# Kernel optimization log

Hardware: AMD Instinct MI355X
Metric: run time of the kernel (lower is better)

The kernel has to match this reference:

```python
import jax, jax.numpy as jnp
import numpy as np

B, T, C, H = 8, 1024, 1024, 16
NEG = -1000000000.0
EPS = 1e-12


def setup_inputs() -> dict:
    key = jax.random.key(0)
    ks = jax.random.split(key, 12)
    s = 0.02  # keep pre-softmax logits in a sane range
    return {
        "x": jax.random.normal(ks[0], (B, T, C), jnp.float32),
        "mask": jax.random.randint(ks[1], (B, T), 0, 2, jnp.int32),
        "Wq": jax.random.normal(ks[2], (C, C), jnp.float32) * s,
        "bq": jax.random.normal(ks[3], (C,), jnp.float32) * s,
        "Wk": jax.random.normal(ks[4], (C, C), jnp.float32) * s,
        "bk": jax.random.normal(ks[5], (C,), jnp.float32) * s,
        "Wv": jax.random.normal(ks[6], (C, C), jnp.float32) * s,
        "bv": jax.random.normal(ks[7], (C,), jnp.float32) * s,
        "Wp": jax.random.normal(ks[8], (C, C), jnp.float32) * s,
        "bp": jax.random.normal(ks[9], (C,), jnp.float32) * s,
        "ln_w": jnp.ones((C,), jnp.float32),
        "ln_b": jnp.zeros((C,), jnp.float32),
    }


def reference(x, mask, Wq, bq, Wk, bk, Wv, bv, Wp, bp, ln_w, ln_b):
    Bx, Tx, Cx = x.shape
    hd = Cx // H
    # torch nn.Linear: y = x @ W.T + b
    def lin(inp, W, b):
        return inp @ W.T + b

    def split_heads(t):  # [B,T,C] -> [B,H,T,hd]
        return t.reshape(Bx, Tx, H, hd).transpose(0, 2, 1, 3)

    q = split_heads(lin(x, Wq, bq))
    k = split_heads(lin(x, Wk, bk))
    v = split_heads(lin(x, Wv, bv))

    att = jnp.einsum("bhqd,bhkd->bhqk", q, k) * (1.0 / jnp.sqrt(jnp.float32(hd)))
    # mask [B,T] masks key positions; broadcast to [B,1,1,T]
    att = jnp.where(mask[:, None, None, :] == 0, NEG, att)
    # stable softmax (manual max-subtract, matching original)
    att = jax.nn.softmax(att, axis=-1)
    # dropout prob 0.0 -> identity (eval-mode faithful)
    y = jnp.einsum("bhqk,bhkd->bhqd", att, v)
    y = y.transpose(0, 2, 1, 3).reshape(Bx, Tx, Cx)
    y = lin(y, Wp, bp)
    # residual + LayerNorm(eps=1e-12)
    z = y + x
    mu = jnp.mean(z, axis=-1, keepdims=True)
    var = jnp.mean(jnp.square(z - mu), axis=-1, keepdims=True)
    out = (z - mu) * jax.lax.rsqrt(var + EPS) * ln_w + ln_b
    return out
```

## Files before the change

### kernel.cpp

```cpp
#include <hip/hip_runtime.h>
#include <stdint.h>

#define B_ 8
#define T_ 1024
#define C_ 1024
#define H_ 16
#define HD 64
#define M_TOT (B_ * T_)

using f32x4 = __attribute__((ext_vector_type(4))) float;
using s16x8 = __attribute__((ext_vector_type(8))) short;
using i32x4 = __attribute__((ext_vector_type(4))) int;

__device__ __forceinline__ unsigned short f2bf(float f) {
  unsigned int u = __builtin_bit_cast(unsigned int, f);
  unsigned int r = (u + 0x7fffu + ((u >> 16) & 1u)) >> 16;
  return (unsigned short)r;
}

__device__ __forceinline__ void gload_lds16(const void* g, void* l) {
  __builtin_amdgcn_global_load_lds(
      (const __attribute__((address_space(1))) unsigned int*)g,
      (__attribute__((address_space(3))) unsigned int*)l, 16, 0, 0);
}

__global__ __launch_bounds__(256) void k_convert(
    const float* __restrict__ x, const float* __restrict__ wq,
    const float* __restrict__ wk, const float* __restrict__ wv,
    const float* __restrict__ wp, const float* __restrict__ bq,
    const float* __restrict__ bk, const float* __restrict__ bv,
    const int* __restrict__ maskp, unsigned short* __restrict__ xb,
    unsigned short* __restrict__ wqkv, unsigned short* __restrict__ wpb,
    float* __restrict__ bias_cat, unsigned int* __restrict__ mpair) {
  const long n_x = (long)M_TOT * C_;
  const long W_ELT = (long)C_ * C_;
  const long total4 = (n_x + 4 * W_ELT) >> 2;
  for (long i4 = (long)blockIdx.x * blockDim.x + threadIdx.x; i4 < total4;
       i4 += (long)gridDim.x * blockDim.x) {
    long i = i4 << 2;
    const float* src;
    unsigned short* dst;
    if (i < n_x) {
      src = x + i;
      dst = xb + i;
    } else {
      long off = i - n_x;
      int which = (int)(off >> 20);
      long wo = off & (W_ELT - 1);
      if (which < 3) {
        src = (which == 0 ? wq : which == 1 ? wk : wv) + wo;
        dst = wqkv + which * W_ELT + wo;
      } else {
        src = wp + wo;
        dst = wpb + wo;
      }
    }
    float4 v = *(const float4*)src;
    ushort4 u;
    u.x = f2bf(v.x); u.y = f2bf(v.y); u.z = f2bf(v.z); u.w = f2bf(v.w);
    *(ushort4*)dst = u;
  }
  int t = blockIdx.x * blockDim.x + threadIdx.x;
  if (t < 3 * C_) {
    float v = t < C_ ? bq[t] : (t < 2 * C_ ? bk[t - C_] : bv[t - 2 * C_]);
    bias_cat[t] = v;
  }
  if (t < B_ * T_ / 2) {
    const int* mr = maskp + t * 2;
    mpair[t] = (mr[0] ? 0xFFFFu : 0u) | (mr[1] ? 0xFFFF0000u : 0u);
  }
}

template <int EPI>
__global__ __launch_bounds__(256, 2) void k_gemm(
    const unsigned short* __restrict__ A, const unsigned short* __restrict__ Bm,
    const float* __restrict__ bias, unsigned short* __restrict__ q_ws,
    unsigned short* __restrict__ k_ws, unsigned short* __restrict__ vt_ws,
    const float* __restrict__ xres, float* __restrict__ zout) {
  __shared__ unsigned short Al[2][128 * 64];
  __shared__ unsigned short Bl[2][128 * 64];
  const int tid = threadIdx.x, lane = tid & 63, w = tid >> 6;
  const int lc = lane & 15, lr = lane >> 4;
  const int wm = w >> 1, wn = w & 1;
  const int GX = (EPI == 0) ? 24 : 8;
  const int NWG = GX * 64;
  int flat = blockIdx.y * GX + blockIdx.x;
  int swz = (flat & 7) * (NWG / 8) + (flat >> 3);
  const int m0 = (swz / GX) * 128, n0 = (swz % GX) * 128;
  const char* Ab = (const char*)A;
  const char* Bb = (const char*)Bm;

  f32x4 acc[4][4] = {};

  auto stage = [&](int buf, int kt) {
#pragma unroll
    for (int i = 0; i < 4; ++i) {
      int g = i * 256 + tid;
      int row = g >> 3, gr = g & 7;
      gload_lds16(Ab + (long)(m0 + row) * 2048 + kt * 128 + ((gr ^ (row & 7)) << 4),
                  (char*)Al[buf] + (i * 256 + w * 64) * 16);
    }
#pragma unroll
    for (int i = 0; i < 4; ++i) {
      int g = i * 256 + tid;
      int row = g >> 3, gr = g & 7;
      gload_lds16(Bb + (long)(n0 + row) * 2048 + kt * 128 + ((gr ^ (row & 7)) << 4),
                  (char*)Bl[buf] + (i * 256 + w * 64) * 16);
    }
  };

  stage(0, 0);
  stage(1, 1);
  asm volatile("s_waitcnt vmcnt(8)" ::: "memory");
  __builtin_amdgcn_sched_barrier(0);
  __builtin_amdgcn_s_barrier();
  __builtin_amdgcn_sched_barrier(0);

#pragma unroll
  for (int kt = 0; kt < 16; ++kt) {
    const int cur = kt & 1;
    const char* Ac = (const char*)Al[cur];
    const char* Bc = (const char*)Bl[cur];
    s16x8 af0[4], bf0[4];
#pragma unroll
    for (int mf = 0; mf < 4; ++mf) {
      int ar = wm * 64 + mf * 16 + lc;
      af0[mf] = *(const s16x8*)(Ac + ar * 128 + ((lr ^ (ar & 7)) << 4));
    }
#pragma unroll
    for (int nf = 0; nf < 4; ++nf) {
      int br = wn * 64 + nf * 16 + lc;
      bf0[nf] = *(const s16x8*)(Bc + br * 128 + ((lr ^ (br & 7)) << 4));
    }
#pragma unroll
    for (int mf = 0; mf < 4; ++mf)
#pragma unroll
      for (int nf = 0; nf < 4; ++nf)
        acc[mf][nf] = __builtin_amdgcn_mfma_f32_16x16x32_bf16(af0[mf], bf0[nf],
                                                              acc[mf][nf], 0, 0, 0);
    s16x8 af1[4], bf1[4];
#pragma unroll
    for (int mf = 0; mf < 4; ++mf) {
      int ar = wm * 64 + mf * 16 + lc;
      af1[mf] = *(const s16x8*)(Ac + ar * 128 + (((4 + lr) ^ (ar & 7)) << 4));
    }
#pragma unroll
    for (int nf = 0; nf < 4; ++nf) {
      int br = wn * 64 + nf * 16 + lc;
      bf1[nf] = *(const s16x8*)(Bc + br * 128 + (((4 + lr) ^ (br & 7)) << 4));
    }
    asm volatile("s_waitcnt lgkmcnt(0)" ::: "memory");
    __builtin_amdgcn_sched_barrier(0);
    __builtin_amdgcn_s_barrier();
    __builtin_amdgcn_sched_barrier(0);
    if (kt + 2 < 16) stage(cur, kt + 2);
    __builtin_amdgcn_s_setprio(1);
#pragma unroll
    for (int mf = 0; mf < 4; ++mf)
#pragma unroll
      for (int nf = 0; nf < 4; ++nf)
        acc[mf][nf] = __builtin_amdgcn_mfma_f32_16x16x32_bf16(af1[mf], bf1[nf],
                                                              acc[mf][nf], 0, 0, 0);
    __builtin_amdgcn_s_setprio(0);
    if (kt + 2 < 16)
      asm volatile("s_waitcnt vmcnt(8)" ::: "memory");
    else
      asm volatile("s_waitcnt vmcnt(0)" ::: "memory");
    __builtin_amdgcn_sched_barrier(0);
    __builtin_amdgcn_s_barrier();
    __builtin_amdgcn_sched_barrier(0);
  }

  if (EPI == 0) {
#pragma unroll
    for (int mf = 0; mf < 4; ++mf)
#pragma unroll
      for (int nf = 0; nf < 4; ++nf) {
        int gn = n0 + wn * 64 + nf * 16 + lc;
        int which = gn >> 10, nn = gn & 1023;
        int hh = nn >> 6, dd = nn & 63;
        float bia = bias[gn];
        if (which == 2) {
          int gm = m0 + wm * 64 + mf * 16 + lr * 4;
          int bb = gm >> 10, tt = gm & 1023;
          ushort4 pk;
          pk.x = f2bf(acc[mf][nf][0] + bia);
          pk.y = f2bf(acc[mf][nf][1] + bia);
          pk.z = f2bf(acc[mf][nf][2] + bia);
          pk.w = f2bf(acc[mf][nf][3] + bia);
          *(ushort4*)&vt_ws[((long)(bb * H_ + hh) * HD + dd) * T_ + tt] = pk;
        } else {
          unsigned short* dst = (which == 0) ? q_ws : k_ws;
          float scl = (which == 0) ? 0.18033688011112042f : 1.0f;
#pragma unroll
          for (int i = 0; i < 4; ++i) {
            int gm = m0 + wm * 64 + mf * 16 + lr * 4 + i;
            int bb = gm >> 10, tt = gm & 1023;
            dst[((long)(bb * H_ + hh) * T_ + tt) * HD + dd] =
                f2bf((acc[mf][nf][i] + bia) * scl);
          }
        }
      }
  } else {
#pragma unroll
    for (int mf = 0; mf < 4; ++mf)
#pragma unroll
      for (int nf = 0; nf < 4; ++nf) {
        int gn = n0 + wn * 64 + nf * 16 + lc;
        float bia = bias[gn];
#pragma unroll
        for (int i = 0; i < 4; ++i) {
          int gm = m0 + wm * 64 + mf * 16 + lr * 4 + i;
          long idx = (long)gm * C_ + gn;
          zout[idx] = acc[mf][nf][i] + bia + xres[idx];
        }
      }
  }
}

__global__ __launch_bounds__(512, 4) void k_attn(
    const unsigned short* __restrict__ Qp, const unsigned short* __restrict__ Kp,
    const unsigned short* __restrict__ Vtp, const unsigned int* __restrict__ mpairp,
    unsigned short* __restrict__ Yp) {
  __shared__ unsigned short Kl[2][64 * 64];
  __shared__ unsigned short Vl[2][64 * 64];
  const int tid = threadIdx.x, lane = tid & 63, w = tid >> 6;
  const int bid = blockIdx.x;
  const int xcd = bid & 7, slot = bid >> 3;
  const int bh = xcd * 16 + (slot >> 3);
  const int qt = slot & 7;
  const int b = bh >> 4, h = bh & 15;
  const int lc = lane & 15, lr = lane >> 4;
  const int q0 = qt * 128 + w * 16;

  const unsigned short* qbase = Qp + ((long)bh * T_ + q0) * HD;
  s16x8 aq0 = *(const s16x8*)(qbase + lc * HD + lr * 8);
  s16x8 aq1 = *(const s16x8*)(qbase + lc * HD + 32 + lr * 8);

  s16x8 ones;
#pragma unroll
  for (int j = 0; j < 8; ++j) ones[j] = (short)0x3F80;

  f32x4 o[4] = {};
  f32x4 o_l = {};

  const char* kb_g = (const char*)(Kp + (long)bh * T_ * HD);
  const char* vb_g = (const char*)(Vtp + (long)bh * HD * T_);
  const unsigned int* mrow2 = mpairp + b * (T_ / 2);

  auto stage = [&](int buf, int kt) {
    int f = tid * 16;
    int row = f >> 7;
    int swz = (f & 127) ^ ((row & 7) << 4);
    gload_lds16(kb_g + (long)kt * 8192 + (f & ~127) + swz,
                (char*)Kl[buf] + w * 1024);
    gload_lds16(vb_g + (long)row * (T_ * 2) + kt * 128 + swz,
                (char*)Vl[buf] + w * 1024);
  };

  stage(0, 0);
  __syncthreads();

  const int s01 = lc + ((lane & 16) << 1);
  const int s23 = s01 + 16;
  const bool hi = (lane >= 32);

  int cur = 0;
  for (int kt = 0; kt < T_ / 64; ++kt) {
    if (kt + 1 < T_ / 64) stage(cur ^ 1, kt + 1);

    f32x4 s[4];
    const char* kl = (const char*)Kl[cur];
#pragma unroll
    for (int kf = 0; kf < 4; ++kf) {
      int key = kf * 16 + lc;
      s16x8 kb0 = *(const s16x8*)(kl + ((key * 128 + lr * 16) ^ ((key & 7) << 4)));
      s16x8 kb1 = *(const s16x8*)(kl + ((key * 128 + 64 + lr * 16) ^ ((key & 7) << 4)));
      f32x4 z = {};
      z = __builtin_amdgcn_mfma_f32_16x16x32_bf16(kb0, aq0, z, 0, 0, 0);
      z = __builtin_amdgcn_mfma_f32_16x16x32_bf16(kb1, aq1, z, 0, 0, 0);
      s[kf] = z;
    }

    unsigned int mw[4][2];
#pragma unroll
    for (int kf = 0; kf < 4; ++kf) {
      mw[kf][0] = mrow2[kt * 32 + kf * 8 + lr * 2];
      mw[kf][1] = mrow2[kt * 32 + kf * 8 + lr * 2 + 1];
    }

    unsigned int pk[4][2];
#pragma unroll
    for (int kf = 0; kf < 4; ++kf) {
      float p0 = __builtin_amdgcn_exp2f(s[kf][0]);
      float p1 = __builtin_amdgcn_exp2f(s[kf][1]);
      float p2 = __builtin_amdgcn_exp2f(s[kf][2]);
      float p3 = __builtin_amdgcn_exp2f(s[kf][3]);
      unsigned int u0 = __builtin_bit_cast(unsigned int, p0);
      unsigned int u1 = __builtin_bit_cast(unsigned int, p1);
      unsigned int u2 = __builtin_bit_cast(unsigned int, p2);
      unsigned int u3 = __builtin_bit_cast(unsigned int, p3);
      pk[kf][0] = ((u1 & 0xFFFF0000u) | (u0 >> 16)) & mw[kf][0];
      pk[kf][1] = ((u3 & 0xFFFF0000u) | (u2 >> 16)) & mw[kf][1];
    }

    s16x8 ap[2];
#pragma unroll
    for (int kc = 0; kc < 2; ++kc) {
      unsigned int A0 = pk[kc * 2][0], A1 = pk[kc * 2][1];
      unsigned int B0 = pk[kc * 2 + 1][0], B1 = pk[kc * 2 + 1][1];
      unsigned int w0a = __shfl((int)A0, s01, 64), w0b = __shfl((int)B0, s01, 64);
      unsigned int w1a = __shfl((int)A1, s01, 64), w1b = __shfl((int)B1, s01, 64);
      unsigned int w2a = __shfl((int)A0, s23, 64), w2b = __shfl((int)B0, s23, 64);
      unsigned int w3a = __shfl((int)A1, s23, 64), w3b = __shfl((int)B1, s23, 64);
      i32x4 wv;
      wv[0] = (int)(hi ? w0b : w0a);
      wv[1] = (int)(hi ? w1b : w1a);
      wv[2] = (int)(hi ? w2b : w2a);
      wv[3] = (int)(hi ? w3b : w3a);
      ap[kc] = __builtin_bit_cast(s16x8, wv);
    }

#pragma unroll
    for (int kc = 0; kc < 2; ++kc) {
      int koff = kc * 64 + lr * 16;
      o_l = __builtin_amdgcn_mfma_f32_16x16x32_bf16(ones, ap[kc], o_l, 0, 0, 0);
#pragma unroll
      for (int nf = 0; nf < 4; ++nf) {
        int drow = nf * 16 + lc;
        s16x8 vb = *(const s16x8*)((const char*)Vl[cur] +
                                   ((drow * 128 + koff) ^ ((drow & 7) << 4)));
        o[nf] = __builtin_amdgcn_mfma_f32_16x16x32_bf16(vb, ap[kc], o[nf], 0, 0, 0);
      }
    }
    __syncthreads();
    cur ^= 1;
  }

  float rl = 1.0f / o_l[0];
  unsigned short* yrow = Yp + ((long)(b * T_ + q0 + lc)) * C_ + h * 64;
#pragma unroll
  for (int nf = 0; nf < 4; ++nf) {
    ushort4 pw;
    pw.x = f2bf(o[nf][0] * rl);
    pw.y = f2bf(o[nf][1] * rl);
    pw.z = f2bf(o[nf][2] * rl);
    pw.w = f2bf(o[nf][3] * rl);
    *(ushort4*)(yrow + nf * 16 + lr * 4) = pw;
  }
}

__global__ __launch_bounds__(256) void k_ln(const float* __restrict__ z,
                                            const float* __restrict__ lw,
                                            const float* __restrict__ lb,
                                            float* __restrict__ out) {
  const int row = blockIdx.x;
  float4 v = ((const float4*)(z + (long)row * C_))[threadIdx.x];
  float s = v.x + v.y + v.z + v.w;
  float s2 = v.x * v.x + v.y * v.y + v.z * v.z + v.w * v.w;
#pragma unroll
  for (int d = 1; d < 64; d <<= 1) {
    s += __shfl_xor(s, d, 64);
    s2 += __shfl_xor(s2, d, 64);
  }
  __shared__ float rs[4], rq[4];
  int wv_ = threadIdx.x >> 6;
  if ((threadIdx.x & 63) == 0) { rs[wv_] = s; rq[wv_] = s2; }
  __syncthreads();
  s = rs[0] + rs[1] + rs[2] + rs[3];
  s2 = rq[0] + rq[1] + rq[2] + rq[3];
  float mu = s * (1.0f / C_);
  float var = s2 * (1.0f / C_) - mu * mu;
  float inv = rsqrtf(var + 1e-12f);
  float4 wv4 = ((const float4*)lw)[threadIdx.x];
  float4 bv4 = ((const float4*)lb)[threadIdx.x];
  float4 ov;
  ov.x = (v.x - mu) * inv * wv4.x + bv4.x;
  ov.y = (v.y - mu) * inv * wv4.y + bv4.y;
  ov.z = (v.z - mu) * inv * wv4.z + bv4.z;
  ov.w = (v.w - mu) * inv * wv4.w + bv4.w;
  ((float4*)(out + (long)row * C_))[threadIdx.x] = ov;
}

extern "C" void kernel_launch(void* const* d_in, const int* in_sizes, int n_in,
                              void* d_out, int out_size, void* d_ws,
                              size_t ws_size, hipStream_t stream) {
  const float* x = (const float*)d_in[0];
  const int* mask = (const int*)d_in[1];
  const float* Wq = (const float*)d_in[2];
  const float* bq = (const float*)d_in[3];
  const float* Wk = (const float*)d_in[4];
  const float* bk = (const float*)d_in[5];
  const float* Wv = (const float*)d_in[6];
  const float* bv = (const float*)d_in[7];
  const float* Wp = (const float*)d_in[8];
  const float* bp = (const float*)d_in[9];
  const float* lnw = (const float*)d_in[10];
  const float* lnb = (const float*)d_in[11];
  float* out = (float*)d_out;

  char* ws = (char*)d_ws;
  const size_t MB = 1024 * 1024;
  unsigned short* xb = (unsigned short*)(ws);
  unsigned short* q_ws = (unsigned short*)(ws + 16 * MB);
  unsigned short* k_ws = (unsigned short*)(ws + 32 * MB);
  unsigned short* vt_ws = (unsigned short*)(ws + 48 * MB);
  unsigned short* y_ws = (unsigned short*)(ws + 64 * MB);
  unsigned short* wqkv = (unsigned short*)(ws + 80 * MB);
  unsigned short* wpb = (unsigned short*)(ws + 86 * MB);
  float* bias_cat = (float*)(ws + 88 * MB);
  unsigned int* mpair = (unsigned int*)(ws + 88 * MB + 16384);
  float* z = (float*)(ws);

  k_convert<<<dim3(2048), dim3(256), 0, stream>>>(x, Wq, Wk, Wv, Wp, bq, bk, bv,
                                                  mask, xb, wqkv, wpb, bias_cat,
                                                  mpair);
  k_gemm<0><<<dim3(24, 64), dim3(256), 0, stream>>>(
      xb, wqkv, bias_cat, q_ws, k_ws, vt_ws, nullptr, nullptr);
  k_attn<<<dim3(1024), dim3(512), 0, stream>>>(q_ws, k_ws, vt_ws, mpair, y_ws);
  k_gemm<1><<<dim3(8, 64), dim3(256), 0, stream>>>(
      y_ws, wpb, bp, nullptr, nullptr, nullptr, x, z);
  k_ln<<<dim3(8192), dim3(256), 0, stream>>>(z, lnw, lnb, out);
}
```

Measured before the change: 176.2 us.

## Give each attention wave four query tiles and store the residual sum in bf16

The attention kernel now runs 256-thread blocks in which each wave handles 64 queries (four 16-row groups) instead of 16. Each K/V fragment read from LDS is reused across four MFMAs, halving the number of blocks and cutting LDS traffic per FLOP; s_setprio is added around the PV MFMAs. Separately, the output projection reads the bf16 copy of x as the residual and writes z in bf16, and the LayerNorm reads bf16, halving residual and z memory traffic. This costs more registers per wave (lower occupancy) and rounds the pre-LayerNorm values to bf16, which reduces accuracy.

```diff
diff --git a/kernel.cpp b/kernel.cpp
--- a/kernel.cpp
+++ b/kernel.cpp
@@ -16,6 +16,10 @@
   unsigned int u = __builtin_bit_cast(unsigned int, f);
   unsigned int r = (u + 0x7fffu + ((u >> 16) & 1u)) >> 16;
   return (unsigned short)r;
+}
+__device__ __forceinline__ float bf2f(unsigned short s) {
+  unsigned int u = ((unsigned int)s) << 16;
+  return __builtin_bit_cast(float, u);
 }
 
 __device__ __forceinline__ void gload_lds16(const void* g, void* l) {
@@ -76,7 +80,7 @@
     const unsigned short* __restrict__ A, const unsigned short* __restrict__ Bm,
     const float* __restrict__ bias, unsigned short* __restrict__ q_ws,
     unsigned short* __restrict__ k_ws, unsigned short* __restrict__ vt_ws,
-    const float* __restrict__ xres, float* __restrict__ zout) {
+    const unsigned short* __restrict__ xres16, unsigned short* __restrict__ z16) {
   __shared__ unsigned short Al[2][128 * 64];
   __shared__ unsigned short Bl[2][128 * 64];
   const int tid = threadIdx.x, lane = tid & 63, w = tid >> 6;
@@ -212,13 +216,13 @@
         for (int i = 0; i < 4; ++i) {
           int gm = m0 + wm * 64 + mf * 16 + lr * 4 + i;
           long idx = (long)gm * C_ + gn;
-          zout[idx] = acc[mf][nf][i] + bia + xres[idx];
+          z16[idx] = f2bf(acc[mf][nf][i] + bia + bf2f(xres16[idx]));
         }
       }
   }
 }
 
-__global__ __launch_bounds__(512, 4) void k_attn(
+__global__ __launch_bounds__(256, 2) void k_attn(
     const unsigned short* __restrict__ Qp, const unsigned short* __restrict__ Kp,
     const unsigned short* __restrict__ Vtp, const unsigned int* __restrict__ mpairp,
     unsigned short* __restrict__ Yp) {
@@ -227,35 +231,42 @@
   const int tid = threadIdx.x, lane = tid & 63, w = tid >> 6;
   const int bid = blockIdx.x;
   const int xcd = bid & 7, slot = bid >> 3;
-  const int bh = xcd * 16 + (slot >> 3);
-  const int qt = slot & 7;
+  const int bh = xcd * 16 + (slot >> 2);
+  const int qt = slot & 3;
   const int b = bh >> 4, h = bh & 15;
   const int lc = lane & 15, lr = lane >> 4;
-  const int q0 = qt * 128 + w * 16;
+  const int q0 = qt * 256 + w * 64;
 
   const unsigned short* qbase = Qp + ((long)bh * T_ + q0) * HD;
-  s16x8 aq0 = *(const s16x8*)(qbase + lc * HD + lr * 8);
-  s16x8 aq1 = *(const s16x8*)(qbase + lc * HD + 32 + lr * 8);
+  s16x8 aq[4][2];
+#pragma unroll
+  for (int g = 0; g < 4; ++g) {
+    aq[g][0] = *(const s16x8*)(qbase + (g * 16 + lc) * HD + lr * 8);
+    aq[g][1] = *(const s16x8*)(qbase + (g * 16 + lc) * HD + 32 + lr * 8);
+  }
 
   s16x8 ones;
 #pragma unroll
   for (int j = 0; j < 8; ++j) ones[j] = (short)0x3F80;
 
-  f32x4 o[4] = {};
-  f32x4 o_l = {};
+  f32x4 o[4][4] = {};
+  f32x4 ol[4] = {};
 
   const char* kb_g = (const char*)(Kp + (long)bh * T_ * HD);
   const char* vb_g = (const char*)(Vtp + (long)bh * HD * T_);
   const unsigned int* mrow2 = mpairp + b * (T_ / 2);
 
   auto stage = [&](int buf, int kt) {
-    int f = tid * 16;
-    int row = f >> 7;
-    int swz = (f & 127) ^ ((row & 7) << 4);
-    gload_lds16(kb_g + (long)kt * 8192 + (f & ~127) + swz,
-                (char*)Kl[buf] + w * 1024);
-    gload_lds16(vb_g + (long)row * (T_ * 2) + kt * 128 + swz,
-                (char*)Vl[buf] + w * 1024);
+#pragma unroll
+    for (int it = 0; it < 2; ++it) {
+      int f = it * 4096 + w * 1024 + lane * 16;
+      int row = f >> 7;
+      int swz = (f & 127) ^ ((row & 7) << 4);
+      gload_lds16(kb_g + (long)kt * 8192 + (f & ~127) + swz,
+                  (char*)Kl[buf] + it * 4096 + w * 1024);
+      gload_lds16(vb_g + (long)row * (T_ * 2) + kt * 128 + swz,
+                  (char*)Vl[buf] + it * 4096 + w * 1024);
+    }
   };
 
   stage(0, 0);
@@ -269,17 +280,20 @@
   for (int kt = 0; kt < T_ / 64; ++kt) {
     if (kt + 1 < T_ / 64) stage(cur ^ 1, kt + 1);
 
-    f32x4 s[4];
+    f32x4 s[4][4];
     const char* kl = (const char*)Kl[cur];
 #pragma unroll
     for (int kf = 0; kf < 4; ++kf) {
       int key = kf * 16 + lc;
       s16x8 kb0 = *(const s16x8*)(kl + ((key * 128 + lr * 16) ^ ((key & 7) << 4)));
       s16x8 kb1 = *(const s16x8*)(kl + ((key * 128 + 64 + lr * 16) ^ ((key & 7) << 4)));
-      f32x4 z = {};
-      z = __builtin_amdgcn_mfma_f32_16x16x32_bf16(kb0, aq0, z, 0, 0, 0);
-      z = __builtin_amdgcn_mfma_f32_16x16x32_bf16(kb1, aq1, z, 0, 0, 0);
-      s[kf] = z;
+#pragma unroll
+      for (int g = 0; g < 4; ++g) {
+        f32x4 z = {};
+        z = __builtin_amdgcn_mfma_f32_16x16x32_bf16(kb0, aq[g][0], z, 0, 0, 0);
+        z = __builtin_amdgcn_mfma_f32_16x16x32_bf16(kb1, aq[g][1], z, 0, 0, 0);
+        s[g][kf] = z;
+      }
     }
 
     unsigned int mw[4][2];
@@ -289,73 +303,81 @@
       mw[kf][1] = mrow2[kt * 32 + kf * 8 + lr * 2 + 1];
     }
 
-    unsigned int pk[4][2];
-#pragma unroll
-    for (int kf = 0; kf < 4; ++kf) {
-      float p0 = __builtin_amdgcn_exp2f(s[kf][0]);
-      float p1 = __builtin_amdgcn_exp2f(s[kf][1]);
-      float p2 = __builtin_amdgcn_exp2f(s[kf][2]);
-      float p3 = __builtin_amdgcn_exp2f(s[kf][3]);
-      unsigned int u0 = __builtin_bit_cast(unsigned int, p0);
-      unsigned int u1 = __builtin_bit_cast(unsigned int, p1);
-      unsigned int u2 = __builtin_bit_cast(unsigned int, p2);
-      unsigned int u3 = __builtin_bit_cast(unsigned int, p3);
-      pk[kf][0] = ((u1 & 0xFFFF0000u) | (u0 >> 16)) & mw[kf][0];
-      pk[kf][1] = ((u3 & 0xFFFF0000u) | (u2 >> 16)) & mw[kf][1];
-    }
-
-    s16x8 ap[2];
+    unsigned int pk[4][4][2];
+#pragma unroll
+    for (int g = 0; g < 4; ++g)
+#pragma unroll
+      for (int kf = 0; kf < 4; ++kf) {
+        unsigned int u0 = __builtin_bit_cast(unsigned int, __builtin_amdgcn_exp2f(s[g][kf][0]));
+        unsigned int u1 = __builtin_bit_cast(unsigned int, __builtin_amdgcn_exp2f(s[g][kf][1]));
+        unsigned int u2 = __builtin_bit_cast(unsigned int, __builtin_amdgcn_exp2f(s[g][kf][2]));
+        unsigned int u3 = __builtin_bit_cast(unsigned int, __builtin_amdgcn_exp2f(s[g][kf][3]));
+        pk[g][kf][0] = ((u1 & 0xFFFF0000u) | (u0 >> 16)) & mw[kf][0];
+        pk[g][kf][1] = ((u3 & 0xFFFF0000u) | (u2 >> 16)) & mw[kf][1];
+      }
+
 #pragma unroll
     for (int kc = 0; kc < 2; ++kc) {
-      unsigned int A0 = pk[kc * 2][0], A1 = pk[kc * 2][1];
-      unsigned int B0 = pk[kc * 2 + 1][0], B1 = pk[kc * 2 + 1][1];
-      unsigned int w0a = __shfl((int)A0, s01, 64), w0b = __shfl((int)B0, s01, 64);
-      unsigned int w1a = __shfl((int)A1, s01, 64), w1b = __shfl((int)B1, s01, 64);
-      unsigned int w2a = __shfl((int)A0, s23, 64), w2b = __shfl((int)B0, s23, 64);
-      unsigned int w3a = __shfl((int)A1, s23, 64), w3b = __shfl((int)B1, s23, 64);
-      i32x4 wv;
-      wv[0] = (int)(hi ? w0b : w0a);
-      wv[1] = (int)(hi ? w1b : w1a);
-      wv[2] = (int)(hi ? w2b : w2a);
-      wv[3] = (int)(hi ? w3b : w3a);
-      ap[kc] = __builtin_bit_cast(s16x8, wv);
-    }
-
-#pragma unroll
-    for (int kc = 0; kc < 2; ++kc) {
+      s16x8 ap[4];
+#pragma unroll
+      for (int g = 0; g < 4; ++g) {
+        unsigned int A0 = pk[g][kc * 2][0], A1 = pk[g][kc * 2][1];
+        unsigned int B0 = pk[g][kc * 2 + 1][0], B1 = pk[g][kc * 2 + 1][1];
+        unsigned int w0a = __shfl((int)A0, s01, 64), w0b = __shfl((int)B0, s01, 64);
+        unsigned int w1a = __shfl((int)A1, s01, 64), w1b = __shfl((int)B1, s01, 64);
+        unsigned int w2a = __shfl((int)A0, s23, 64), w2b = __shfl((int)B0, s23, 64);
+        unsigned int w3a = __shfl((int)A1, s23, 64), w3b = __shfl((int)B1, s23, 64);
+        i32x4 wv;
+        wv[0] = (int)(hi ? w0b : w0a);
+        wv[1] = (int)(hi ? w1b : w1a);
+        wv[2] = (int)(hi ? w2b : w2a);
+        wv[3] = (int)(hi ? w3b : w3a);
+        ap[g] = __builtin_bit_cast(s16x8, wv);
+      }
       int koff = kc * 64 + lr * 16;
-      o_l = __builtin_amdgcn_mfma_f32_16x16x32_bf16(ones, ap[kc], o_l, 0, 0, 0);
+      __builtin_amdgcn_s_setprio(1);
+#pragma unroll
+      for (int g = 0; g < 4; ++g)
+        ol[g] = __builtin_amdgcn_mfma_f32_16x16x32_bf16(ones, ap[g], ol[g], 0, 0, 0);
 #pragma unroll
       for (int nf = 0; nf < 4; ++nf) {
         int drow = nf * 16 + lc;
         s16x8 vb = *(const s16x8*)((const char*)Vl[cur] +
                                    ((drow * 128 + koff) ^ ((drow & 7) << 4)));
-        o[nf] = __builtin_amdgcn_mfma_f32_16x16x32_bf16(vb, ap[kc], o[nf], 0, 0, 0);
-      }
+#pragma unroll
+        for (int g = 0; g < 4; ++g)
+          o[g][nf] = __builtin_amdgcn_mfma_f32_16x16x32_bf16(vb, ap[g], o[g][nf], 0, 0, 0);
+      }
+      __builtin_amdgcn_s_setprio(0);
     }
     __syncthreads();
     cur ^= 1;
   }
 
-  float rl = 1.0f / o_l[0];
-  unsigned short* yrow = Yp + ((long)(b * T_ + q0 + lc)) * C_ + h * 64;
-#pragma unroll
-  for (int nf = 0; nf < 4; ++nf) {
-    ushort4 pw;
-    pw.x = f2bf(o[nf][0] * rl);
-    pw.y = f2bf(o[nf][1] * rl);
-    pw.z = f2bf(o[nf][2] * rl);
-    pw.w = f2bf(o[nf][3] * rl);
-    *(ushort4*)(yrow + nf * 16 + lr * 4) = pw;
-  }
-}
-
-__global__ __launch_bounds__(256) void k_ln(const float* __restrict__ z,
+#pragma unroll
+  for (int g = 0; g < 4; ++g) {
+    float rl = 1.0f / ol[g][0];
+    unsigned short* yrow = Yp + ((long)(b * T_ + q0 + g * 16 + lc)) * C_ + h * 64;
+#pragma unroll
+    for (int nf = 0; nf < 4; ++nf) {
+      ushort4 pw;
+      pw.x = f2bf(o[g][nf][0] * rl);
+      pw.y = f2bf(o[g][nf][1] * rl);
+      pw.z = f2bf(o[g][nf][2] * rl);
+      pw.w = f2bf(o[g][nf][3] * rl);
+      *(ushort4*)(yrow + nf * 16 + lr * 4) = pw;
+    }
+  }
+}
+
+__global__ __launch_bounds__(256) void k_ln(const unsigned short* __restrict__ z16,
                                             const float* __restrict__ lw,
                                             const float* __restrict__ lb,
                                             float* __restrict__ out) {
   const int row = blockIdx.x;
-  float4 v = ((const float4*)(z + (long)row * C_))[threadIdx.x];
+  ushort4 v16 = ((const ushort4*)(z16 + (long)row * C_))[threadIdx.x];
+  float4 v;
+  v.x = bf2f(v16.x); v.y = bf2f(v16.y); v.z = bf2f(v16.z); v.w = bf2f(v16.w);
   float s = v.x + v.y + v.z + v.w;
   float s2 = v.x * v.x + v.y * v.y + v.z * v.z + v.w * v.w;
 #pragma unroll
@@ -410,15 +432,15 @@
   unsigned short* wpb = (unsigned short*)(ws + 86 * MB);
   float* bias_cat = (float*)(ws + 88 * MB);
   unsigned int* mpair = (unsigned int*)(ws + 88 * MB + 16384);
-  float* z = (float*)(ws);
+  unsigned short* z16 = (unsigned short*)(ws + 48 * MB);
 
   k_convert<<<dim3(2048), dim3(256), 0, stream>>>(x, Wq, Wk, Wv, Wp, bq, bk, bv,
                                                   mask, xb, wqkv, wpb, bias_cat,
                                                   mpair);
   k_gemm<0><<<dim3(24, 64), dim3(256), 0, stream>>>(
       xb, wqkv, bias_cat, q_ws, k_ws, vt_ws, nullptr, nullptr);
-  k_attn<<<dim3(1024), dim3(512), 0, stream>>>(q_ws, k_ws, vt_ws, mpair, y_ws);
+  k_attn<<<dim3(512), dim3(256), 0, stream>>>(q_ws, k_ws, vt_ws, mpair, y_ws);
   k_gemm<1><<<dim3(8, 64), dim3(256), 0, stream>>>(
-      y_ws, wpb, bp, nullptr, nullptr, nullptr, x, z);
-  k_ln<<<dim3(8192), dim3(256), 0, stream>>>(z, lnw, lnb, out);
-}
+      y_ws, wpb, bp, nullptr, nullptr, nullptr, xb, z16);
+  k_ln<<<dim3(8192), dim3(256), 0, stream>>>(z16, lnw, lnb, out);
+}
```

New measurement: 163.9 us (median of 3 runs). 1.08x faster.
